# Optimization experiments

Measured on AMD Instinct MI355X. Metric: run time of the kernel, lower is better.

Reference implementation:

```python
import jax, jax.numpy as jnp
import numpy as np

B, N, D, H, LH, AH = 4, 2048, 512, 4, 64, 64
NUM_BUCKETS = 128
EPS = 1e-6
LENGTHS = np.array([2048, 1536, 1024, 1792])  # jagged per-sequence lengths, sum = 6400


def _ln(x, eps=EPS):
    # F.layer_norm without affine params (biased variance)
    m = jnp.mean(x, axis=-1, keepdims=True)
    v = jnp.var(x, axis=-1, keepdims=True)
    return (x - m) * jax.lax.rsqrt(v + eps)


def _rel_bias(all_timestamps, ts_w):
    # bucketed time-delta relative attention bias -> [B, N, N]
    delta = (all_timestamps[:, :, None] - all_timestamps[:, None, :]).astype(jnp.float32)
    bucket = jnp.clip(jnp.floor(jnp.log1p(jnp.abs(delta))).astype(jnp.int32), 0, NUM_BUCKETS)
    return ts_w[bucket]


def setup_inputs() -> dict:
    key = jax.random.key(0)
    ks = jax.random.split(key, 6)
    offsets = np.concatenate([[0], np.cumsum(LENGTHS)]).astype(np.int32)
    T = int(offsets[-1])
    token_batch = np.repeat(np.arange(B), LENGTHS).astype(np.int32)
    token_pos = np.concatenate([np.arange(l) for l in LENGTHS]).astype(np.int32)
    x = jax.random.normal(ks[0], (T, D), jnp.float32)
    uvqk = jax.random.normal(ks[1], (D, 2 * LH * H + 2 * AH * H), jnp.float32) * 0.02
    o_w = jax.random.normal(ks[2], (D, LH * H), jnp.float32) * 0.02  # torch Linear weight [out, in]
    o_b = jnp.zeros((D,), jnp.float32)
    ts_w = jax.random.normal(ks[3], (NUM_BUCKETS + 1,), jnp.float32) * 0.02
    all_timestamps = jnp.sort(jax.random.randint(ks[4], (B, N), 0, 1000000, jnp.int32), axis=-1)
    invalid_attn_mask = jnp.tril(jnp.ones((N, N), jnp.float32))  # causal validity mask in {0,1}
    return {
        'x': x, 'uvqk': uvqk, 'o_w': o_w, 'o_b': o_b, 'ts_w': ts_w,
        'all_timestamps': all_timestamps, 'invalid_attn_mask': invalid_attn_mask,
        'x_offsets': jnp.asarray(offsets), 'token_batch': jnp.asarray(token_batch),
        'token_pos': jnp.asarray(token_pos),
    }


def reference(x, uvqk, o_w, o_b, ts_w, all_timestamps, invalid_attn_mask,
              x_offsets, token_batch, token_pos):
    # input layernorm + fused uvqk projection with SiLU
    h = jax.nn.silu(_ln(x) @ uvqk)  # [T, 2*H*LH + 2*H*AH]
    u, v, q, k = jnp.split(h, [LH * H, 2 * LH * H, 2 * LH * H + AH * H], axis=1)

    def pad(vals):  # jagged [T, d] -> padded dense [B, N, d]
        return jnp.zeros((B, N, vals.shape[-1]), vals.dtype).at[token_batch, token_pos].set(vals)

    pq = pad(q).reshape(B, N, H, AH)
    pk = pad(k).reshape(B, N, H, AH)
    pv = pad(v).reshape(B, N, H, LH)

    scores = jnp.einsum('bnhd,bmhd->bhnm', pq, pk)
    scores = scores + _rel_bias(all_timestamps, ts_w)[:, None]  # broadcast over heads
    scores = jax.nn.silu(scores) / N
    scores = scores * invalid_attn_mask[None, None]
    attn = jnp.einsum('bhnm,bmhd->bnhd', scores, pv).reshape(B, N, H * LH)
    attn_j = attn[token_batch, token_pos]  # dense -> jagged [T, H*LH]

    o_in = u * _ln(attn_j)
    return o_in @ o_w.T + o_b + x
```

## Files before the change

### kernel.cpp

```cpp
#include <hip/hip_runtime.h>
#include <math.h>


typedef __attribute__((ext_vector_type(8))) short bf16x8;
typedef __attribute__((ext_vector_type(4))) float f32x4;

__device__ __forceinline__ float silu_over_2048(float v) {
    return v * __builtin_amdgcn_rcpf(2048.0f + 2048.0f * __expf(-v));
}

__device__ __forceinline__ float silu_f(float v) {
    return v * __builtin_amdgcn_rcpf(1.0f + __expf(-v));
}

__device__ __forceinline__ unsigned short f2bf(float f) {
    unsigned int u = __float_as_uint(f);
    u += 0x7fffu + ((u >> 16) & 1u);
    return (unsigned short)(u >> 16);
}

__device__ __forceinline__ unsigned int f2bf2(float lo, float hi) {
#if __has_builtin(__builtin_amdgcn_cvt_pk_bf16_f32)
    typedef __attribute__((ext_vector_type(2))) short bf16x2;
    bf16x2 p = __builtin_amdgcn_cvt_pk_bf16_f32(lo, hi);
    return *(unsigned int*)&p;
#else
    return (unsigned int)f2bf(lo) | ((unsigned int)f2bf(hi) << 16);
#endif
}

__global__ __launch_bounds__(256) void k1_ln_prep(const float* __restrict__ x,
                                                  unsigned short* __restrict__ xnb,
                                                  const float* __restrict__ uvqk,
                                                  unsigned short* __restrict__ uvqkT,
                                                  const float* __restrict__ ow,
                                                  unsigned short* __restrict__ owb) {
    const int tid = threadIdx.x;
    const int bx = blockIdx.x;
    if (bx < 1600) {
        const int row = bx * 4 + (tid >> 6);
        const int lane = tid & 63;
        const float* xr = x + row * 512 + lane * 8;
        const float4 v0 = *(const float4*)xr;
        const float4 v1 = *(const float4*)(xr + 4);
        float s = v0.x + v0.y + v0.z + v0.w + v1.x + v1.y + v1.z + v1.w;
        float ss = v0.x * v0.x + v0.y * v0.y + v0.z * v0.z + v0.w * v0.w +
                   v1.x * v1.x + v1.y * v1.y + v1.z * v1.z + v1.w * v1.w;
#pragma unroll
        for (int off = 32; off > 0; off >>= 1) {
            s += __shfl_down(s, off);
            ss += __shfl_down(ss, off);
        }
        s = __shfl(s, 0);
        ss = __shfl(ss, 0);
        const float mean = s * (1.0f / 512.0f);
        const float var = ss * (1.0f / 512.0f) - mean * mean;
        const float rstd = rsqrtf(var + 1e-6f);
        unsigned int pk[4];
        pk[0] = f2bf2((v0.x - mean) * rstd, (v0.y - mean) * rstd);
        pk[1] = f2bf2((v0.z - mean) * rstd, (v0.w - mean) * rstd);
        pk[2] = f2bf2((v1.x - mean) * rstd, (v1.y - mean) * rstd);
        pk[3] = f2bf2((v1.z - mean) * rstd, (v1.w - mean) * rstd);
        *(uint4*)(xnb + row * 512 + lane * 8) = *(const uint4*)pk;
    } else if (bx < 1728) {
        __shared__ float L[64][68];
        const int t = bx - 1600;
        const int n0 = (t & 15) * 64;
        const int k0 = (t >> 4) * 64;
#pragma unroll
        for (int i = 0; i < 4; ++i) {
            const int r = (tid >> 4) + i * 16;
            const int c = (tid & 15) * 4;
            *(float4*)&L[r][c] = *(const float4*)(uvqk + (k0 + r) * 1024 + n0 + c);
        }
        __syncthreads();
        const int n = tid >> 2;
        const int kb = (tid & 3) * 16;
#pragma unroll
        for (int pass = 0; pass < 2; ++pass) {
            unsigned short pk[8];
#pragma unroll
            for (int j = 0; j < 8; ++j) pk[j] = f2bf(L[kb + pass * 8 + j][n]);
            *(uint4*)(uvqkT + (n0 + n) * 512 + k0 + kb + pass * 8) = *(const uint4*)pk;
        }
    } else {
        const int base = ((bx - 1728) * 256 + tid) * 8;
        float4 a = *(const float4*)(ow + base);
        float4 b = *(const float4*)(ow + base + 4);
        unsigned short pk[8] = {f2bf(a.x), f2bf(a.y), f2bf(a.z), f2bf(a.w),
                                f2bf(b.x), f2bf(b.y), f2bf(b.z), f2bf(b.w)};
        *(uint4*)(owb + base) = *(const uint4*)pk;
    }
}

__global__ __launch_bounds__(256, 4) void k2_gemm1(const unsigned short* __restrict__ A,
                                                   const unsigned short* __restrict__ Bt,
                                                   float* __restrict__ u_out,
                                                   unsigned short* __restrict__ hb,
                                                   unsigned short* __restrict__ vtb) {
    __shared__ __align__(16) unsigned short As[64][72];
    __shared__ __align__(16) unsigned short Bs[64][72];
    const int tid = threadIdx.x;
    const int lane = tid & 63;
    const int w = tid >> 6;
    const int l15 = lane & 15;
    const int quad = lane >> 4;
    const int bm = blockIdx.y * 64;
    const int bn = blockIdx.x * 64;

    f32x4 acc[4] = {};
    for (int kc = 0; kc < 512; kc += 64) {
        __syncthreads();
#pragma unroll
        for (int i = 0; i < 2; ++i) {
            const int r = (tid >> 3) + i * 32;
            const int c = (tid & 7) * 8;
            *(uint4*)&As[r][c] = *(const uint4*)(A + (bm + r) * 512 + kc + c);
            *(uint4*)&Bs[r][c] = *(const uint4*)(Bt + (bn + r) * 512 + kc + c);
        }
        __syncthreads();
        const bf16x8 a0 = *(const bf16x8*)&As[w * 16 + l15][quad * 8];
        const bf16x8 a1 = *(const bf16x8*)&As[w * 16 + l15][32 + quad * 8];
#pragma unroll
        for (int nt = 0; nt < 4; ++nt) {
            bf16x8 b0 = *(const bf16x8*)&Bs[nt * 16 + l15][quad * 8];
            bf16x8 b1 = *(const bf16x8*)&Bs[nt * 16 + l15][32 + quad * 8];
            acc[nt] = __builtin_amdgcn_mfma_f32_16x16x32_bf16(a0, b0, acc[nt], 0, 0, 0);
            acc[nt] = __builtin_amdgcn_mfma_f32_16x16x32_bf16(a1, b1, acc[nt], 0, 0, 0);
        }
    }
    const int m = bm + w * 16 + quad * 4;
    if (bn < 256) {
#pragma unroll
        for (int nt = 0; nt < 4; ++nt)
#pragma unroll
            for (int reg = 0; reg < 4; ++reg)
                u_out[(m + reg) * 256 + bn + nt * 16 + l15] = silu_f(acc[nt][reg]);
    } else if (bn < 512) {
        __syncthreads();
#pragma unroll
        for (int nt = 0; nt < 4; ++nt) {
            unsigned int p01 = f2bf2(silu_f(acc[nt][0]), silu_f(acc[nt][1]));
            unsigned int p23 = f2bf2(silu_f(acc[nt][2]), silu_f(acc[nt][3]));
            unsigned int pk2[2] = {p01, p23};
            *(uint2*)&As[nt * 16 + l15][w * 16 + quad * 4] = *(const uint2*)pk2;
        }
        __syncthreads();
        const int sr = tid >> 3, sc = (tid & 7) * 8;
#pragma unroll
        for (int i = 0; i < 2; ++i) {
            const int r = sr + i * 32;
            *(uint4*)(vtb + (size_t)(bn - 256 + r) * 6400 + bm + sc) =
                *(const uint4*)&As[r][sc];
        }
    } else {
#pragma unroll
        for (int nt = 0; nt < 4; ++nt) {
            unsigned int p01 = f2bf2(silu_f(acc[nt][0]), silu_f(acc[nt][1]));
            unsigned int p23 = f2bf2(silu_f(acc[nt][2]), silu_f(acc[nt][3]));
            unsigned short* hp = hb + (size_t)m * 768 + (bn - 256) + nt * 16 + l15;
            hp[0] = (unsigned short)p01;
            hp[768] = (unsigned short)(p01 >> 16);
            hp[1536] = (unsigned short)p23;
            hp[2304] = (unsigned short)(p23 >> 16);
        }
    }
}

__global__ __launch_bounds__(256, 5) void k3_attn(const unsigned short* __restrict__ hb,
                                                  const unsigned short* __restrict__ vtb,
                                                  const int* __restrict__ ts,
                                                  const float* __restrict__ tsw,
                                                  const int* __restrict__ offs,
                                                  float* __restrict__ part) {
    const int qt = 31 - (blockIdx.x & 31);
    const int c = blockIdx.x >> 5;
    const int b = blockIdx.y;
    const int hd = blockIdx.z;
    const int off = offs[b];
    const int len = offs[b + 1] - off;
    const int nqt = len >> 6;
    if (qt >= nqt || c * 4 > qt) return;
    const int q0 = qt * 64;
    const int kt_lo = c * 4;
    const int kt_hi = min(qt, c * 4 + 3);

    __shared__ __align__(16) unsigned short QPs[64][72];
    __shared__ __align__(16) unsigned short Ks[64][72];
    __shared__ __align__(16) unsigned short Vt[64][72];
    __shared__ float tqf[64], tkf[64];
    __shared__ float tw[132];

    const int tid = threadIdx.x;
    const int lane = tid & 63;
    const int w = tid >> 6;
    const int l15 = lane & 15;
    const int quad = lane >> 4;
    const int sr = tid >> 3;
    const int sc = (tid & 7) * 8;

    if (tid < 129) tw[tid] = tsw[tid];
    if (tid < 64) tqf[tid] = (float)ts[b * 2048 + q0 + tid];
#pragma unroll
    for (int i = 0; i < 2; ++i)
        *(uint4*)&QPs[sr + i * 32][sc] =
            *(const uint4*)(hb + (off + q0 + sr + i * 32) * 768 + 256 + hd * 64 + sc);
    __syncthreads();

    const bf16x8 aQ0 = *(const bf16x8*)&QPs[w * 16 + l15][quad * 8];
    const bf16x8 aQ1 = *(const bf16x8*)&QPs[w * 16 + l15][32 + quad * 8];
    const f32x4 tq4 = *(const f32x4*)&tqf[w * 16 + quad * 4];
    const int nbase = q0 + w * 16 + quad * 4;

    f32x4 oacc[4] = {};

    for (int kt = kt_lo; kt <= kt_hi; ++kt) {
        const int m0 = kt * 64;
        __syncthreads();
#pragma unroll
        for (int i = 0; i < 2; ++i) {
            const int r = sr + i * 32;
            *(uint4*)&Ks[r][sc] =
                *(const uint4*)(hb + (off + m0 + r) * 768 + 512 + hd * 64 + sc);
            *(uint4*)&Vt[r][sc] =
                *(const uint4*)(vtb + (size_t)(hd * 64 + r) * 6400 + off + m0 + sc);
        }
        if (tid < 64) tkf[tid] = (float)ts[b * 2048 + m0 + tid];
        __syncthreads();

        f32x4 s[4] = {};
#pragma unroll
        for (int nt = 0; nt < 4; ++nt) {
            bf16x8 b0 = *(const bf16x8*)&Ks[nt * 16 + l15][quad * 8];
            bf16x8 b1 = *(const bf16x8*)&Ks[nt * 16 + l15][32 + quad * 8];
            s[nt] = __builtin_amdgcn_mfma_f32_16x16x32_bf16(aQ0, b0, s[nt], 0, 0, 0);
            s[nt] = __builtin_amdgcn_mfma_f32_16x16x32_bf16(aQ1, b1, s[nt], 0, 0, 0);
        }

        const bool diag = (kt == qt);
#pragma unroll
        for (int nt = 0; nt < 4; ++nt) {
            const int m = m0 + nt * 16 + l15;
            const float tk = tkf[nt * 16 + l15];
            float p[4];
#pragma unroll
            for (int reg = 0; reg < 4; ++reg) {
                const float delta = fabsf(tq4[reg] - tk);
                const int bucket = (int)(__log2f(1.0f + delta) * 0.6931471805599453f);
                float val = s[nt][reg] + tw[bucket];
                float pv = silu_over_2048(val);
                if (diag) pv = (m <= nbase + reg) ? pv : 0.0f;
                p[reg] = pv;
            }
            const unsigned int p01 = f2bf2(p[0], p[1]);
            const unsigned int p23 = f2bf2(p[2], p[3]);
            QPs[w * 16 + quad * 4 + 0][nt * 16 + l15] = (unsigned short)p01;
            QPs[w * 16 + quad * 4 + 1][nt * 16 + l15] = (unsigned short)(p01 >> 16);
            QPs[w * 16 + quad * 4 + 2][nt * 16 + l15] = (unsigned short)p23;
            QPs[w * 16 + quad * 4 + 3][nt * 16 + l15] = (unsigned short)(p23 >> 16);
        }

        const bf16x8 aP0 = *(const bf16x8*)&QPs[w * 16 + l15][quad * 8];
        const bf16x8 aP1 = *(const bf16x8*)&QPs[w * 16 + l15][32 + quad * 8];
#pragma unroll
        for (int nt = 0; nt < 4; ++nt) {
            bf16x8 v0 = *(const bf16x8*)&Vt[nt * 16 + l15][quad * 8];
            bf16x8 v1 = *(const bf16x8*)&Vt[nt * 16 + l15][32 + quad * 8];
            oacc[nt] = __builtin_amdgcn_mfma_f32_16x16x32_bf16(aP0, v0, oacc[nt], 0, 0, 0);
            oacc[nt] = __builtin_amdgcn_mfma_f32_16x16x32_bf16(aP1, v1, oacc[nt], 0, 0, 0);
        }
    }

    float* pc = part + (size_t)c * (6400 * 256);
#pragma unroll
    for (int nt = 0; nt < 4; ++nt)
#pragma unroll
        for (int reg = 0; reg < 4; ++reg)
            pc[(off + q0 + w * 16 + quad * 4 + reg) * 256 + hd * 64 + nt * 16 + l15] =
                oacc[nt][reg];
}

__global__ __launch_bounds__(256) void k4a_ln(const float* __restrict__ part,
                                              const float* __restrict__ u_in,
                                              const int* __restrict__ token_pos,
                                              unsigned short* __restrict__ o_in) {
    const int row = blockIdx.x;
    const int tid = threadIdx.x;
    const int qt = token_pos[row] >> 6;
    const int nch = (qt + 4) >> 2;
    float a = 0.0f;
    for (int c = 0; c < nch; ++c) a += part[(size_t)c * (6400 * 256) + row * 256 + tid];
    float s = a, ss = a * a;
#pragma unroll
    for (int off = 32; off > 0; off >>= 1) {
        s += __shfl_down(s, off);
        ss += __shfl_down(ss, off);
    }
    __shared__ float red[8];
    if ((tid & 63) == 0) { red[tid >> 6] = s; red[4 + (tid >> 6)] = ss; }
    __syncthreads();
    s = red[0] + red[1] + red[2] + red[3];
    ss = red[4] + red[5] + red[6] + red[7];
    const float mean = s * (1.0f / 256.0f);
    const float var = ss * (1.0f / 256.0f) - mean * mean;
    const float rstd = rsqrtf(var + 1e-6f);
    const float u = u_in[row * 256 + tid];
    o_in[row * 256 + tid] = f2bf(u * (a - mean) * rstd);
}

__global__ __launch_bounds__(256, 4) void k4b_gemm2(const unsigned short* __restrict__ A,
                                                    const unsigned short* __restrict__ owb,
                                                    const float* __restrict__ ob,
                                                    const float* __restrict__ x,
                                                    float* __restrict__ out) {
    __shared__ __align__(16) unsigned short As[64][72];
    __shared__ __align__(16) unsigned short Bs[64][72];
    const int tid = threadIdx.x;
    const int lane = tid & 63;
    const int w = tid >> 6;
    const int l15 = lane & 15;
    const int quad = lane >> 4;
    const int bm = blockIdx.y * 64;
    const int bn = blockIdx.x * 64;

    f32x4 acc[4] = {};
    for (int kc = 0; kc < 256; kc += 64) {
        __syncthreads();
#pragma unroll
        for (int i = 0; i < 2; ++i) {
            const int r = (tid >> 3) + i * 32;
            const int c = (tid & 7) * 8;
            *(uint4*)&As[r][c] = *(const uint4*)(A + (bm + r) * 256 + kc + c);
            *(uint4*)&Bs[r][c] = *(const uint4*)(owb + (bn + r) * 256 + kc + c);
        }
        __syncthreads();
        const bf16x8 a0 = *(const bf16x8*)&As[w * 16 + l15][quad * 8];
        const bf16x8 a1 = *(const bf16x8*)&As[w * 16 + l15][32 + quad * 8];
#pragma unroll
        for (int nt = 0; nt < 4; ++nt) {
            bf16x8 b0 = *(const bf16x8*)&Bs[nt * 16 + l15][quad * 8];
            bf16x8 b1 = *(const bf16x8*)&Bs[nt * 16 + l15][32 + quad * 8];
            acc[nt] = __builtin_amdgcn_mfma_f32_16x16x32_bf16(a0, b0, acc[nt], 0, 0, 0);
            acc[nt] = __builtin_amdgcn_mfma_f32_16x16x32_bf16(a1, b1, acc[nt], 0, 0, 0);
        }
    }
    const int m = bm + w * 16 + quad * 4;
#pragma unroll
    for (int nt = 0; nt < 4; ++nt) {
        const int d = bn + nt * 16 + l15;
        const float bias = ob[d];
#pragma unroll
        for (int reg = 0; reg < 4; ++reg)
            out[(m + reg) * 512 + d] = acc[nt][reg] + bias + x[(m + reg) * 512 + d];
    }
}

extern "C" void kernel_launch(void* const* d_in, const int* in_sizes, int n_in,
                              void* d_out, int out_size, void* d_ws, size_t ws_size,
                              hipStream_t stream) {
    const float* x = (const float*)d_in[0];
    const float* uvqk = (const float*)d_in[1];
    const float* ow = (const float*)d_in[2];
    const float* ob = (const float*)d_in[3];
    const float* tsw = (const float*)d_in[4];
    const int* ts = (const int*)d_in[5];
    const int* offs = (const int*)d_in[7];
    const int* token_pos = (const int*)d_in[9];
    float* out = (float*)d_out;

    float* ws = (float*)d_ws;
    float* u = ws;
    float* part = u + 6400 * 256;
    unsigned short* xnb = (unsigned short*)(part + 8 * 6400 * 256);
    unsigned short* hb = xnb + 6400 * 512;
    unsigned short* o_in = hb + 6400 * 768;
    unsigned short* uvqkT = o_in + 6400 * 256;
    unsigned short* owb = uvqkT + 1024 * 512;
    unsigned short* vtb = owb + 512 * 256;

    k1_ln_prep<<<1792, 256, 0, stream>>>(x, xnb, uvqk, uvqkT, ow, owb);
    k2_gemm1<<<dim3(16, 100), 256, 0, stream>>>(xnb, uvqkT, u, hb, vtb);
    k3_attn<<<dim3(256, 4, 4), 256, 0, stream>>>(hb, vtb, ts, tsw, offs, part);
    k4a_ln<<<6400, 256, 0, stream>>>(part, u, token_pos, o_in);
    k4b_gemm2<<<dim3(8, 100), 256, 0, stream>>>(o_in, owb, ob, x, out);
}
```

Baseline: 160.3 us.

## Retile both bf16 GEMMs to 128x128 blocks with direct global-to-LDS loads

Both projection GEMMs move from 64x64 tiles with one 16-row strip per wave to 128x128 tiles. Waves sit in a 2x2 grid, and each wave computes a 4x4 set of 16x16 MFMA tiles, so every LDS fragment it reads is reused across four MFMAs. Operand staging now uses global_load_lds, writing directly into unpadded LDS instead of going through registers. The V-transpose epilogue is reworked to write two 64-column halves through a padded LDS tile. In exchange, far fewer blocks are launched (200 for the output GEMM), which may underfill the GPU. The unpadded 64-element LDS rows may also cause bank conflicts on fragment reads.

```diff
diff --git a/kernel.cpp b/kernel.cpp
--- a/kernel.cpp
+++ b/kernel.cpp
@@ -27,6 +27,13 @@
 #else
     return (unsigned int)f2bf(lo) | ((unsigned int)f2bf(hi) << 16);
 #endif
+}
+
+__device__ __forceinline__ void gload_lds16(const unsigned short* g, unsigned short* l) {
+    __builtin_amdgcn_global_load_lds(
+        (const __attribute__((address_space(1))) void*)(g),
+        (__attribute__((address_space(3))) void*)(l),
+        16, 0, 0);
 }
 
 __global__ __launch_bounds__(256) void k1_ln_prep(const float* __restrict__ x,
@@ -93,77 +100,108 @@
     }
 }
 
-__global__ __launch_bounds__(256, 4) void k2_gemm1(const unsigned short* __restrict__ A,
-                                                   const unsigned short* __restrict__ Bt,
-                                                   float* __restrict__ u_out,
-                                                   unsigned short* __restrict__ hb,
-                                                   unsigned short* __restrict__ vtb) {
-    __shared__ __align__(16) unsigned short As[64][72];
-    __shared__ __align__(16) unsigned short Bs[64][72];
+__global__ __launch_bounds__(256) void k2_gemm1(const unsigned short* __restrict__ A,
+                                                const unsigned short* __restrict__ Bt,
+                                                float* __restrict__ u_out,
+                                                unsigned short* __restrict__ hb,
+                                                unsigned short* __restrict__ vtb) {
+    __shared__ __align__(16) unsigned short smem[16384];
+    unsigned short* As = smem;
+    unsigned short* Bs = smem + 8192;
     const int tid = threadIdx.x;
     const int lane = tid & 63;
     const int w = tid >> 6;
     const int l15 = lane & 15;
     const int quad = lane >> 4;
-    const int bm = blockIdx.y * 64;
-    const int bn = blockIdx.x * 64;
-
-    f32x4 acc[4] = {};
+    const int wr = w >> 1;
+    const int wc = w & 1;
+    const int bm = blockIdx.y * 128;
+    const int bn = blockIdx.x * 128;
+
+    const int srow = lane >> 3;
+    const int scol = (lane & 7) * 8;
+    const unsigned short* gA = A + (size_t)(bm + w * 8 + srow) * 512 + scol;
+    const unsigned short* gB = Bt + (size_t)(bn + w * 8 + srow) * 512 + scol;
+
+    f32x4 acc[4][4] = {};
     for (int kc = 0; kc < 512; kc += 64) {
         __syncthreads();
 #pragma unroll
-        for (int i = 0; i < 2; ++i) {
-            const int r = (tid >> 3) + i * 32;
-            const int c = (tid & 7) * 8;
-            *(uint4*)&As[r][c] = *(const uint4*)(A + (bm + r) * 512 + kc + c);
-            *(uint4*)&Bs[r][c] = *(const uint4*)(Bt + (bn + r) * 512 + kc + c);
-        }
-        __syncthreads();
-        const bf16x8 a0 = *(const bf16x8*)&As[w * 16 + l15][quad * 8];
-        const bf16x8 a1 = *(const bf16x8*)&As[w * 16 + l15][32 + quad * 8];
-#pragma unroll
-        for (int nt = 0; nt < 4; ++nt) {
-            bf16x8 b0 = *(const bf16x8*)&Bs[nt * 16 + l15][quad * 8];
-            bf16x8 b1 = *(const bf16x8*)&Bs[nt * 16 + l15][32 + quad * 8];
-            acc[nt] = __builtin_amdgcn_mfma_f32_16x16x32_bf16(a0, b0, acc[nt], 0, 0, 0);
-            acc[nt] = __builtin_amdgcn_mfma_f32_16x16x32_bf16(a1, b1, acc[nt], 0, 0, 0);
-        }
-    }
-    const int m = bm + w * 16 + quad * 4;
+        for (int i = 0; i < 4; ++i) {
+            gload_lds16(gA + (size_t)(i * 32) * 512 + kc, As + (i * 4 + w) * 512);
+            gload_lds16(gB + (size_t)(i * 32) * 512 + kc, Bs + (i * 4 + w) * 512);
+        }
+        __syncthreads();
+#pragma unroll
+        for (int kk = 0; kk < 2; ++kk) {
+            bf16x8 a[4], b[4];
+#pragma unroll
+            for (int mi = 0; mi < 4; ++mi)
+                a[mi] = *(const bf16x8*)&As[(wr * 64 + mi * 16 + l15) * 64 + kk * 32 + quad * 8];
+#pragma unroll
+            for (int ni = 0; ni < 4; ++ni)
+                b[ni] = *(const bf16x8*)&Bs[(wc * 64 + ni * 16 + l15) * 64 + kk * 32 + quad * 8];
+#pragma unroll
+            for (int mi = 0; mi < 4; ++mi)
+#pragma unroll
+                for (int ni = 0; ni < 4; ++ni)
+                    acc[mi][ni] =
+                        __builtin_amdgcn_mfma_f32_16x16x32_bf16(a[mi], b[ni], acc[mi][ni], 0, 0, 0);
+        }
+    }
+
+    const int mrow = bm + wr * 64 + quad * 4;
     if (bn < 256) {
 #pragma unroll
-        for (int nt = 0; nt < 4; ++nt)
-#pragma unroll
-            for (int reg = 0; reg < 4; ++reg)
-                u_out[(m + reg) * 256 + bn + nt * 16 + l15] = silu_f(acc[nt][reg]);
+        for (int mi = 0; mi < 4; ++mi)
+#pragma unroll
+            for (int ni = 0; ni < 4; ++ni) {
+                float* up = u_out + (size_t)(mrow + mi * 16) * 256 + bn + wc * 64 + ni * 16 + l15;
+#pragma unroll
+                for (int reg = 0; reg < 4; ++reg)
+                    up[reg * 256] = silu_f(acc[mi][ni][reg]);
+            }
     } else if (bn < 512) {
-        __syncthreads();
-#pragma unroll
-        for (int nt = 0; nt < 4; ++nt) {
-            unsigned int p01 = f2bf2(silu_f(acc[nt][0]), silu_f(acc[nt][1]));
-            unsigned int p23 = f2bf2(silu_f(acc[nt][2]), silu_f(acc[nt][3]));
-            unsigned int pk2[2] = {p01, p23};
-            *(uint2*)&As[nt * 16 + l15][w * 16 + quad * 4] = *(const uint2*)pk2;
-        }
-        __syncthreads();
-        const int sr = tid >> 3, sc = (tid & 7) * 8;
-#pragma unroll
-        for (int i = 0; i < 2; ++i) {
-            const int r = sr + i * 32;
-            *(uint4*)(vtb + (size_t)(bn - 256 + r) * 6400 + bm + sc) =
-                *(const uint4*)&As[r][sc];
+        unsigned short(*T)[136] = (unsigned short(*)[136])smem;
+        __syncthreads();
+#pragma unroll
+        for (int h = 0; h < 2; ++h) {
+            if (wc == h) {
+#pragma unroll
+                for (int ni = 0; ni < 4; ++ni)
+#pragma unroll
+                    for (int mi = 0; mi < 4; ++mi) {
+                        unsigned int p01 = f2bf2(silu_f(acc[mi][ni][0]), silu_f(acc[mi][ni][1]));
+                        unsigned int p23 = f2bf2(silu_f(acc[mi][ni][2]), silu_f(acc[mi][ni][3]));
+                        unsigned int pk2[2] = {p01, p23};
+                        *(uint2*)&T[ni * 16 + l15][wr * 64 + mi * 16 + quad * 4] =
+                            *(const uint2*)pk2;
+                    }
+            }
+            __syncthreads();
+#pragma unroll
+            for (int i = 0; i < 4; ++i) {
+                const int r = (tid >> 4) + i * 16;
+                const int cgrp = (tid & 15) * 8;
+                *(uint4*)(vtb + (size_t)(bn - 256 + h * 64 + r) * 6400 + bm + cgrp) =
+                    *(const uint4*)&T[r][cgrp];
+            }
+            __syncthreads();
         }
     } else {
 #pragma unroll
-        for (int nt = 0; nt < 4; ++nt) {
-            unsigned int p01 = f2bf2(silu_f(acc[nt][0]), silu_f(acc[nt][1]));
-            unsigned int p23 = f2bf2(silu_f(acc[nt][2]), silu_f(acc[nt][3]));
-            unsigned short* hp = hb + (size_t)m * 768 + (bn - 256) + nt * 16 + l15;
-            hp[0] = (unsigned short)p01;
-            hp[768] = (unsigned short)(p01 >> 16);
-            hp[1536] = (unsigned short)p23;
-            hp[2304] = (unsigned short)(p23 >> 16);
-        }
+        for (int mi = 0; mi < 4; ++mi)
+#pragma unroll
+            for (int ni = 0; ni < 4; ++ni) {
+                unsigned int p01 = f2bf2(silu_f(acc[mi][ni][0]), silu_f(acc[mi][ni][1]));
+                unsigned int p23 = f2bf2(silu_f(acc[mi][ni][2]), silu_f(acc[mi][ni][3]));
+                unsigned short* hp = hb + (size_t)(mrow + mi * 16) * 768 + (bn - 256) +
+                                     wc * 64 + ni * 16 + l15;
+                hp[0] = (unsigned short)p01;
+                hp[768] = (unsigned short)(p01 >> 16);
+                hp[1536] = (unsigned short)p23;
+                hp[2304] = (unsigned short)(p23 >> 16);
+            }
     }
 }
 
@@ -308,51 +346,68 @@
     o_in[row * 256 + tid] = f2bf(u * (a - mean) * rstd);
 }
 
-__global__ __launch_bounds__(256, 4) void k4b_gemm2(const unsigned short* __restrict__ A,
-                                                    const unsigned short* __restrict__ owb,
-                                                    const float* __restrict__ ob,
-                                                    const float* __restrict__ x,
-                                                    float* __restrict__ out) {
-    __shared__ __align__(16) unsigned short As[64][72];
-    __shared__ __align__(16) unsigned short Bs[64][72];
+__global__ __launch_bounds__(256) void k4b_gemm2(const unsigned short* __restrict__ A,
+                                                 const unsigned short* __restrict__ owb,
+                                                 const float* __restrict__ ob,
+                                                 const float* __restrict__ x,
+                                                 float* __restrict__ out) {
+    __shared__ __align__(16) unsigned short smem[16384];
+    unsigned short* As = smem;
+    unsigned short* Bs = smem + 8192;
     const int tid = threadIdx.x;
     const int lane = tid & 63;
     const int w = tid >> 6;
     const int l15 = lane & 15;
     const int quad = lane >> 4;
-    const int bm = blockIdx.y * 64;
-    const int bn = blockIdx.x * 64;
-
-    f32x4 acc[4] = {};
+    const int wr = w >> 1;
+    const int wc = w & 1;
+    const int bm = blockIdx.y * 128;
+    const int bn = blockIdx.x * 128;
+
+    const int srow = lane >> 3;
+    const int scol = (lane & 7) * 8;
+    const unsigned short* gA = A + (size_t)(bm + w * 8 + srow) * 256 + scol;
+    const unsigned short* gB = owb + (size_t)(bn + w * 8 + srow) * 256 + scol;
+
+    f32x4 acc[4][4] = {};
     for (int kc = 0; kc < 256; kc += 64) {
         __syncthreads();
 #pragma unroll
-        for (int i = 0; i < 2; ++i) {
-            const int r = (tid >> 3) + i * 32;
-            const int c = (tid & 7) * 8;
-            *(uint4*)&As[r][c] = *(const uint4*)(A + (bm + r) * 256 + kc + c);
-            *(uint4*)&Bs[r][c] = *(const uint4*)(owb + (bn + r) * 256 + kc + c);
-        }
-        __syncthreads();
-        const bf16x8 a0 = *(const bf16x8*)&As[w * 16 + l15][quad * 8];
-        const bf16x8 a1 = *(const bf16x8*)&As[w * 16 + l15][32 + quad * 8];
-#pragma unroll
-        for (int nt = 0; nt < 4; ++nt) {
-            bf16x8 b0 = *(const bf16x8*)&Bs[nt * 16 + l15][quad * 8];
-            bf16x8 b1 = *(const bf16x8*)&Bs[nt * 16 + l15][32 + quad * 8];
-            acc[nt] = __builtin_amdgcn_mfma_f32_16x16x32_bf16(a0, b0, acc[nt], 0, 0, 0);
-            acc[nt] = __builtin_amdgcn_mfma_f32_16x16x32_bf16(a1, b1, acc[nt], 0, 0, 0);
-        }
-    }
-    const int m = bm + w * 16 + quad * 4;
-#pragma unroll
-    for (int nt = 0; nt < 4; ++nt) {
-        const int d = bn + nt * 16 + l15;
-        const float bias = ob[d];
-#pragma unroll
-        for (int reg = 0; reg < 4; ++reg)
-            out[(m + reg) * 512 + d] = acc[nt][reg] + bias + x[(m + reg) * 512 + d];
-    }
+        for (int i = 0; i < 4; ++i) {
+            gload_lds16(gA + (size_t)(i * 32) * 256 + kc, As + (i * 4 + w) * 512);
+            gload_lds16(gB + (size_t)(i * 32) * 256 + kc, Bs + (i * 4 + w) * 512);
+        }
+        __syncthreads();
+#pragma unroll
+        for (int kk = 0; kk < 2; ++kk) {
+            bf16x8 a[4], b[4];
+#pragma unroll
+            for (int mi = 0; mi < 4; ++mi)
+                a[mi] = *(const bf16x8*)&As[(wr * 64 + mi * 16 + l15) * 64 + kk * 32 + quad * 8];
+#pragma unroll
+            for (int ni = 0; ni < 4; ++ni)
+                b[ni] = *(const bf16x8*)&Bs[(wc * 64 + ni * 16 + l15) * 64 + kk * 32 + quad * 8];
+#pragma unroll
+            for (int mi = 0; mi < 4; ++mi)
+#pragma unroll
+                for (int ni = 0; ni < 4; ++ni)
+                    acc[mi][ni] =
+                        __builtin_amdgcn_mfma_f32_16x16x32_bf16(a[mi], b[ni], acc[mi][ni], 0, 0, 0);
+        }
+    }
+    const int mrow = bm + wr * 64 + quad * 4;
+#pragma unroll
+    for (int mi = 0; mi < 4; ++mi)
+#pragma unroll
+        for (int ni = 0; ni < 4; ++ni) {
+            const int d = bn + wc * 64 + ni * 16 + l15;
+            const float bias = ob[d];
+            const int m = mrow + mi * 16;
+#pragma unroll
+            for (int reg = 0; reg < 4; ++reg)
+                out[(size_t)(m + reg) * 512 + d] =
+                    acc[mi][ni][reg] + bias + x[(size_t)(m + reg) * 512 + d];
+        }
 }
 
 extern "C" void kernel_launch(void* const* d_in, const int* in_sizes, int n_in,
@@ -379,8 +434,8 @@
     unsigned short* vtb = owb + 512 * 256;
 
     k1_ln_prep<<<1792, 256, 0, stream>>>(x, xnb, uvqk, uvqkT, ow, owb);
-    k2_gemm1<<<dim3(16, 100), 256, 0, stream>>>(xnb, uvqkT, u, hb, vtb);
+    k2_gemm1<<<dim3(8, 50), 256, 0, stream>>>(xnb, uvqkT, u, hb, vtb);
     k3_attn<<<dim3(256, 4, 4), 256, 0, stream>>>(hb, vtb, ts, tsw, offs, part);
     k4a_ln<<<6400, 256, 0, stream>>>(part, u, token_pos, o_in);
-    k4b_gemm2<<<dim3(8, 100), 256, 0, stream>>>(o_in, owb, ob, x, out);
-}
+    k4b_gemm2<<<dim3(4, 50), 256, 0, stream>>>(o_in, owb, ob, x, out);
+}
```

New measurement: 174.4 us. +8.8%, slower.
